# Performance work log

Hardware: AMD Instinct MI355X
Metric: run time of the kernel (lower is better)

The kernel has to match this reference:

```python
import jax, jax.numpy as jnp
import numpy as np

D_MODEL = 1024
NUM_HEADS = 16
HEAD_DIM = D_MODEL // NUM_HEADS
BATCH = 2
SEQ = 2048


def setup_inputs() -> dict:
    key = jax.random.key(0)
    ks = jax.random.split(key, 9)
    s = 1.0 / np.sqrt(D_MODEL)
    inp = {
        "x": jax.random.normal(ks[0], (BATCH, SEQ, D_MODEL), dtype=jnp.float32),
        "mask": jnp.ones((BATCH, SEQ), dtype=jnp.int32),
        "Wq": jax.random.uniform(ks[1], (D_MODEL, D_MODEL), jnp.float32, -s, s),
        "bq": jax.random.uniform(ks[2], (D_MODEL,), jnp.float32, -s, s),
        "Wk": jax.random.uniform(ks[3], (D_MODEL, D_MODEL), jnp.float32, -s, s),
        "bk": jax.random.uniform(ks[4], (D_MODEL,), jnp.float32, -s, s),
        "Wv": jax.random.uniform(ks[5], (D_MODEL, D_MODEL), jnp.float32, -s, s),
        "bv": jax.random.uniform(ks[6], (D_MODEL,), jnp.float32, -s, s),
        "Wo": jax.random.uniform(ks[7], (D_MODEL, D_MODEL), jnp.float32, -s, s),
        "bo": jax.random.uniform(ks[8], (D_MODEL,), jnp.float32, -s, s),
    }
    return inp


def reference(x, mask, Wq, bq, Wk, bk, Wv, bv, Wo, bo):
    B, S, D = x.shape
    H, Hd = NUM_HEADS, HEAD_DIM
    # torch Linear: y = x @ W.T + b ; then reshape to [B, H, S, Hd]
    def proj(W, b):
        return (x @ W.T + b).reshape(B, S, H, Hd).transpose(0, 2, 1, 3)
    Q = proj(Wq, bq)
    K = proj(Wk, bk)
    V = proj(Wv, bv)
    scale = 1.0 / jnp.sqrt(jnp.asarray(Hd, dtype=x.dtype))
    scores = jnp.einsum("bhqd,bhkd->bhqk", Q, K) * scale  # [B,H,S,S]
    # mask [B,S] -> broadcast over query positions; masked_fill(mask==0, -1e9)
    scores = jnp.where(mask[:, None, None, :] == 0, jnp.asarray(-1e9, x.dtype), scores)
    attn = jax.nn.softmax(scores, axis=-1)
    context = jnp.einsum("bhqk,bhkd->bhqd", attn, V)
    context = context.transpose(0, 2, 1, 3).reshape(B, S, D)
    return context @ Wo.T + bo
```

## Files before the change

kernel.cpp:

```cpp
#include <hip/hip_runtime.h>
#include <hip/hip_bf16.h>
#include <cstdint>

#define D_MODEL 1024
#define NUM_HEADS 16
#define HEAD_DIM 64
#define BATCH 2
#define SEQ 2048
#define MROWS (BATCH * SEQ)

typedef __attribute__((ext_vector_type(8))) short bf16x8;
typedef __attribute__((ext_vector_type(4))) float f32x4;
typedef unsigned short u16;

#define QSCALE (0.125f * 1.44269504f)

#if __has_builtin(__builtin_amdgcn_exp2f)
#define EXP2F(x) __builtin_amdgcn_exp2f(x)
#else
#define EXP2F(x) exp2f(x)
#endif

static __device__ __forceinline__ u16 f2bf(float f) {
    unsigned int u = __float_as_uint(f);
    unsigned int lsb = (u >> 16) & 1u;
    u += 0x7fffu + lsb;
    return (u16)(u >> 16);
}

#if __has_builtin(__builtin_amdgcn_cvt_pk_bf16_f32)
static __device__ __forceinline__ unsigned pkbf(float a, float b) {
    typedef __attribute__((ext_vector_type(2))) __bf16 bf2;
    union { bf2 v; unsigned u; } cv;
    cv.v = __builtin_amdgcn_cvt_pk_bf16_f32(a, b);
    return cv.u;
}
#else
static __device__ __forceinline__ unsigned pkbf(float a, float b) {
    unsigned ua = (__float_as_uint(a) + 0x8000u) >> 16;
    unsigned ub = (__float_as_uint(b) + 0x8000u) & 0xffff0000u;
    return ua | ub;
}
#endif

static __device__ __forceinline__ void gload_lds16(const void* g, void* l) {
    __builtin_amdgcn_global_load_lds((const __attribute__((address_space(1))) unsigned int*)g,
                                     (__attribute__((address_space(3))) unsigned int*)l,
                                     16, 0, 0);
}

__global__ void cvt_bf16(const float* __restrict__ src,
                         u16* __restrict__ dst, int n) {
    int i = (blockIdx.x * blockDim.x + threadIdx.x) * 4;
    if (i + 3 < n) {
        float4 v = *(const float4*)(src + i);
        ushort4 o;
        o.x = f2bf(v.x); o.y = f2bf(v.y); o.z = f2bf(v.z); o.w = f2bf(v.w);
        *(ushort4*)(dst + i) = o;
    }
}

__global__ void cvt_bf16_4(const float* __restrict__ s0, const float* __restrict__ s1,
                           const float* __restrict__ s2, const float* __restrict__ s3,
                           u16* __restrict__ dst, int n_each) {
    const int which = blockIdx.y;
    const float* s = (which == 0) ? s0 : (which == 1) ? s1 : (which == 2) ? s2 : s3;
    int i = (blockIdx.x * blockDim.x + threadIdx.x) * 4;
    if (i + 3 < n_each) {
        float4 v = *(const float4*)(s + i);
        ushort4 o;
        o.x = f2bf(v.x); o.y = f2bf(v.y); o.z = f2bf(v.z); o.w = f2bf(v.w);
        *(ushort4*)(dst + (size_t)which * n_each + i) = o;
    }
}

template<int BN, int MODE>
__global__ __launch_bounds__(256, 3)
void gemm_staged(const u16* __restrict__ A, const u16* __restrict__ W,
                 const float* __restrict__ b0, const float* __restrict__ b1,
                 const float* __restrict__ b2,
                 u16* __restrict__ o0, u16* __restrict__ o1, u16* __restrict__ o2,
                 float* __restrict__ of, int K, int N) {
    constexpr int WN = BN / 2;
    constexpr int NJ = WN / 16;
    __shared__ __align__(16) u16 As[128 * 64];
    __shared__ __align__(16) u16 Bs[BN * 64];

    const int lane = threadIdx.x & 63;
    const int w    = threadIdx.x >> 6;
    const int quad = lane >> 4;
    const int l16  = lane & 15;
    const int wm = w >> 1, wn = w & 1;

    const u16* Ablk = A + (size_t)(blockIdx.y * 128) * K;
    const u16* Wblk = W + (size_t)(blockIdx.x * BN) * K;

    const int srow = lane >> 3;
    const int scol = lane & 7;

    f32x4 acc[4][NJ];
#pragma unroll
    for (int i = 0; i < 4; ++i)
#pragma unroll
        for (int j = 0; j < NJ; ++j) acc[i][j] = (f32x4){0.f, 0.f, 0.f, 0.f};

    for (int kb0 = 0; kb0 < K; kb0 += 64) {
        __syncthreads();
#pragma unroll
        for (int t = 0; t < 4; ++t) {
            const int r  = w * 32 + t * 8 + srow;
            const int cg = scol ^ (r & 7);
            gload_lds16(Ablk + (size_t)r * K + kb0 + cg * 8, &As[(w * 32 + t * 8) * 64]);
        }
#pragma unroll
        for (int t = 0; t < BN / 32; ++t) {
            const int r  = w * (BN / 4) + t * 8 + srow;
            const int cg = scol ^ (r & 7);
            gload_lds16(Wblk + (size_t)r * K + kb0 + cg * 8, &Bs[(w * (BN / 4) + t * 8) * 64]);
        }
        __syncthreads();
#pragma unroll
        for (int ks = 0; ks < 2; ++ks) {
            bf16x8 a[4], b[NJ];
#pragma unroll
            for (int i = 0; i < 4; ++i) {
                const int ra = wm * 64 + 16 * i + l16;
                a[i] = *(const bf16x8*)&As[ra * 64 + ((ks * 4 + quad) ^ (ra & 7)) * 8];
            }
#pragma unroll
            for (int j = 0; j < NJ; ++j) {
                const int rb = wn * WN + 16 * j + l16;
                b[j] = *(const bf16x8*)&Bs[rb * 64 + ((ks * 4 + quad) ^ (rb & 7)) * 8];
            }
#pragma unroll
            for (int i = 0; i < 4; ++i)
#pragma unroll
                for (int j = 0; j < NJ; ++j)
                    acc[i][j] = __builtin_amdgcn_mfma_f32_16x16x32_bf16(a[i], b[j], acc[i][j], 0, 0, 0);
        }
    }

    const int mbase = blockIdx.y * 128 + wm * 64;
    const int nbase = blockIdx.x * BN + wn * WN;

    if (MODE == 0) {
#pragma unroll
        for (int j = 0; j < NJ; ++j) {
            const int gn = nbase + 16 * j + l16;
            const int which = gn >> 10, rem = gn & 1023;
            const float bv = (which == 0 ? b0 : which == 1 ? b1 : b2)[rem];
            u16* dst = (which == 0) ? o0 : (which == 1) ? o1 : o2;
            const float scl = (which == 0) ? QSCALE : 1.0f;
            const int h = rem >> 6, d = rem & 63;
#pragma unroll
            for (int i = 0; i < 4; ++i)
#pragma unroll
                for (int r = 0; r < 4; ++r) {
                    const int gm = mbase + 16 * i + quad * 4 + r;
                    const int bb = gm >> 11, s = gm & 2047;
                    dst[(((size_t)(bb * NUM_HEADS + h) * SEQ) + s) * 64 + d] =
                        f2bf((acc[i][j][r] + bv) * scl);
                }
        }
    } else {
#pragma unroll
        for (int j = 0; j < NJ; ++j) {
            const int gn = nbase + 16 * j + l16;
            const float bv = b0[gn];
#pragma unroll
            for (int i = 0; i < 4; ++i)
#pragma unroll
                for (int r = 0; r < 4; ++r) {
                    const int gm = mbase + 16 * i + quad * 4 + r;
                    of[(size_t)gm * N + gn] = acc[i][j][r] + bv;
                }
        }
    }
}

__global__ void transpose_v(const u16* __restrict__ V, u16* __restrict__ VT) {
    __shared__ __align__(16) u16 T[64 * 64];
    const int t    = threadIdx.x;
    const int lane = t & 63, w = t >> 6;
    const int bh   = blockIdx.x & 31, sblk = blockIdx.x >> 5;
    const u16* src = V + ((size_t)bh * SEQ + sblk * 64) * 64;

#pragma unroll
    for (int p = 0; p < 2; ++p) {
        const int r = p * 32 + w * 8 + (lane >> 3);
        const int c = lane & 7;
        bf16x8 v = *(const bf16x8*)(src + r * 64 + c * 8);
        *(bf16x8*)&T[r * 64 + ((c ^ (r & 7)) * 8)] = v;
    }
    __syncthreads();
    u16* dst = VT + ((size_t)bh * 64) * SEQ + sblk * 64;
#pragma unroll
    for (int p = 0; p < 2; ++p) {
        const int r  = p * 32 + w * 8 + (lane >> 3);
        const int sc = lane & 7;
        union { u16 u[8]; bf16x8 v; } pk;
#pragma unroll
        for (int j = 0; j < 8; ++j)
            pk.u[j] = T[(sc * 8 + j) * 64 + (((r >> 3) ^ j) * 8) + (r & 7)];
        *(bf16x8*)(dst + (size_t)r * SEQ + sc * 8) = pk.v;
    }
}

__global__ __launch_bounds__(512, 4)
void attn_kernel(const u16* __restrict__ Q, const u16* __restrict__ K,
                 const u16* __restrict__ VT, const int* __restrict__ mask,
                 u16* __restrict__ ctx) {
    __shared__ __align__(16) u16 Ks[2][64 * 64];
    __shared__ __align__(16) u16 Vs[2][64 * 64];
    __shared__ __align__(16) u16 Ps[8][16 * 72];

    const int lane = threadIdx.x & 63;
    const int w    = threadIdx.x >> 6;
    const int quad = lane >> 4;
    const int l16  = lane & 15;

    const int bh = blockIdx.x & 31;
    const int qb = blockIdx.x >> 5;
    const int b  = bh >> 4;
    const int h  = bh & 15;
    const int qbase = qb * 128 + w * 16;

    const u16* Qh = Q + (size_t)bh * SEQ * 64;
    const u16* Kh = K + (size_t)bh * SEQ * 64;
    const u16* Vh = VT + (size_t)bh * 64 * SEQ;
    const int* mrow = mask + b * SEQ;

    const int srow = lane >> 3;
    const int scol = lane & 7;
    const int cg   = scol ^ srow;

    gload_lds16(Kh + (size_t)(8 * w + srow) * 64 + cg * 8, &Ks[0][(8 * w) * 64]);
    gload_lds16(Vh + (size_t)(8 * w + srow) * SEQ + cg * 8, &Vs[0][(8 * w) * 64]);

    bf16x8 qf[2];
#pragma unroll
    for (int ks = 0; ks < 2; ++ks)
        qf[ks] = *(const bf16x8*)(Qh + (size_t)(qbase + l16) * 64 + 32 * ks + quad * 8);

    f32x4 o[4];
#pragma unroll
    for (int id = 0; id < 4; ++id) o[id] = (f32x4){0.f, 0.f, 0.f, 0.f};
    float lst = 0.f;

    unsigned short* myp = &Ps[w][0];
    const int rowsel = (lane & 48) | (quad * 4);

#pragma unroll 2
    for (int kb = 0; kb < 32; ++kb) {
        const int cur = kb & 1;
        __syncthreads();

        if (kb != 31) {
            const int kn = (kb + 1) * 64;
            gload_lds16(Kh + (size_t)(kn + 8 * w + srow) * 64 + cg * 8,
                        &Ks[cur ^ 1][(8 * w) * 64]);
            gload_lds16(Vh + (size_t)(8 * w + srow) * SEQ + kn + cg * 8,
                        &Vs[cur ^ 1][(8 * w) * 64]);
        }

        const int kstart = kb * 64;
        const int mv = mrow[kstart + lane];
        const bool clean = (__ballot(mv != 0) == ~0ull);

        bf16x8 kf[4][2];
#pragma unroll
        for (int ik = 0; ik < 4; ++ik) {
            const int row = 16 * ik + l16;
#pragma unroll
            for (int ks = 0; ks < 2; ++ks)
                kf[ik][ks] = *(const bf16x8*)&Ks[cur][row * 64 + ((4 * ks + quad) ^ (row & 7)) * 8];
        }

        f32x4 s[4];
#pragma unroll
        for (int ik = 0; ik < 4; ++ik) {
            f32x4 t = (f32x4){0.f, 0.f, 0.f, 0.f};
            t = __builtin_amdgcn_mfma_f32_16x16x32_bf16(kf[ik][0], qf[0], t, 0, 0, 0);
            t = __builtin_amdgcn_mfma_f32_16x16x32_bf16(kf[ik][1], qf[1], t, 0, 0, 0);
            s[ik] = t;
        }

        bf16x8 vf[4][2];
#pragma unroll
        for (int id = 0; id < 4; ++id) {
            const int row = 16 * id + l16;
#pragma unroll
            for (int ks = 0; ks < 2; ++ks)
                vf[id][ks] = *(const bf16x8*)&Vs[cur][row * 64 + ((4 * ks + quad) ^ (row & 7)) * 8];
        }

        if (!clean) {
#pragma unroll
            for (int ik = 0; ik < 4; ++ik) {
                int4 mk = *(const int4*)(mrow + kstart + 16 * ik + quad * 4);
                const int* mp = (const int*)&mk;
#pragma unroll
                for (int r = 0; r < 4; ++r)
                    s[ik][r] = (mp[r] != 0) ? s[ik][r] : -1e9f;
            }
        }

        float rs = 0.f;
#pragma unroll
        for (int ik = 0; ik < 4; ++ik) {
            const float p0 = EXP2F(fminf(s[ik][0], 80.f));
            const float p1 = EXP2F(fminf(s[ik][1], 80.f));
            const float p2 = EXP2F(fminf(s[ik][2], 80.f));
            const float p3 = EXP2F(fminf(s[ik][3], 80.f));
            rs += (p0 + p1) + (p2 + p3);
            uint2 pk;
            pk.x = pkbf(p0, p1);
            pk.y = pkbf(p2, p3);
            *(uint2*)(myp + l16 * 72 + 16 * ik + quad * 4) = pk;
        }
        rs += __shfl_xor(rs, 16, 64);
        rs += __shfl_xor(rs, 32, 64);
        lst += rs;

#pragma unroll
        for (int ks = 0; ks < 2; ++ks) {
            bf16x8 pf = *(const bf16x8*)(myp + l16 * 72 + 32 * ks + quad * 8);
#pragma unroll
            for (int id = 0; id < 4; ++id)
                o[id] = __builtin_amdgcn_mfma_f32_16x16x32_bf16(pf, vf[id][ks], o[id], 0, 0, 0);
        }
    }

    float linv[4];
#pragma unroll
    for (int r = 0; r < 4; ++r) linv[r] = 1.f / __shfl(lst, rowsel + r, 64);
#pragma unroll
    for (int id = 0; id < 4; ++id)
#pragma unroll
        for (int r = 0; r < 4; ++r) {
            const int q = qbase + quad * 4 + r;
            const int d = 16 * id + l16;
            ctx[((size_t)(b * SEQ + q)) * D_MODEL + h * 64 + d] = f2bf(o[id][r] * linv[r]);
        }
}

extern "C" void kernel_launch(void* const* d_in, const int* in_sizes, int n_in,
                              void* d_out, int out_size, void* d_ws, size_t ws_size,
                              hipStream_t stream) {
    const float* x    = (const float*)d_in[0];
    const int*   mask = (const int*)d_in[1];
    const float* Wq   = (const float*)d_in[2];
    const float* bq   = (const float*)d_in[3];
    const float* Wk   = (const float*)d_in[4];
    const float* bk   = (const float*)d_in[5];
    const float* Wv   = (const float*)d_in[6];
    const float* bv   = (const float*)d_in[7];
    const float* Wo   = (const float*)d_in[8];
    const float* bo   = (const float*)d_in[9];

    u16* xb  = (u16*)d_ws;
    u16* wqb = xb  + (size_t)MROWS * D_MODEL;
    u16* wkb = wqb + (size_t)D_MODEL * D_MODEL;
    u16* wvb = wkb + (size_t)D_MODEL * D_MODEL;
    u16* wob = wvb + (size_t)D_MODEL * D_MODEL;
    u16* Qb  = wob + (size_t)D_MODEL * D_MODEL;
    u16* Kb  = Qb  + (size_t)MROWS * D_MODEL;
    u16* VTb = Kb  + (size_t)MROWS * D_MODEL;
    u16* ctx = VTb + (size_t)MROWS * D_MODEL;

    const int nx = MROWS * D_MODEL;
    const int nw = D_MODEL * D_MODEL;
    cvt_bf16<<<nx / 1024, 256, 0, stream>>>(x, xb, nx);
    cvt_bf16_4<<<dim3(nw / 1024, 4), 256, 0, stream>>>(Wq, Wk, Wv, Wo, wqb, nw);

    gemm_staged<128, 0><<<dim3(3 * D_MODEL / 128, MROWS / 128), 256, 0, stream>>>(
        xb, wqb, bq, bk, bv, Qb, Kb, ctx, nullptr, D_MODEL, 3 * D_MODEL);

    transpose_v<<<BATCH * NUM_HEADS * (SEQ / 64), 256, 0, stream>>>(ctx, VTb);

    attn_kernel<<<BATCH * NUM_HEADS * (SEQ / 128), 512, 0, stream>>>(Qb, Kb, VTb, mask, ctx);

    gemm_staged<64, 1><<<dim3(D_MODEL / 64, MROWS / 128), 256, 0, stream>>>(
        ctx, wob, bo, nullptr, nullptr, nullptr, nullptr, nullptr,
        (float*)d_out, D_MODEL, D_MODEL);
}
```

Baseline: 203.6 us.

## Fuse V transpose into QKV GEMM epilogue and merge conversion launches

The QKV projection GEMM now writes V directly in transposed [B,H,D,S] layout by staging the V-tile accumulators through a padded LDS buffer and emitting coalesced 16-byte row stores, which removes the separate transpose_v kernel and its round trip through global memory. The two fp32-to-bf16 conversion kernels are merged into one launch over a 2D grid covering x and all four weight matrices. In exchange, every GEMM instantiation carries an extra 17 KB of shared memory, which may reduce occupancy, and the V blocks add two block-wide barriers to their epilogue.

```diff
diff --git a/kernel.cpp b/kernel.cpp
--- a/kernel.cpp
+++ b/kernel.cpp
@@ -49,29 +49,24 @@
                                      16, 0, 0);
 }
 
-__global__ void cvt_bf16(const float* __restrict__ src,
-                         u16* __restrict__ dst, int n) {
-    int i = (blockIdx.x * blockDim.x + threadIdx.x) * 4;
-    if (i + 3 < n) {
-        float4 v = *(const float4*)(src + i);
-        ushort4 o;
-        o.x = f2bf(v.x); o.y = f2bf(v.y); o.z = f2bf(v.z); o.w = f2bf(v.w);
-        *(ushort4*)(dst + i) = o;
-    }
-}
-
-__global__ void cvt_bf16_4(const float* __restrict__ s0, const float* __restrict__ s1,
-                           const float* __restrict__ s2, const float* __restrict__ s3,
-                           u16* __restrict__ dst, int n_each) {
+__global__ void cvt_all(const float* __restrict__ x,
+                        const float* __restrict__ w0, const float* __restrict__ w1,
+                        const float* __restrict__ w2, const float* __restrict__ w3,
+                        u16* __restrict__ base) {
     const int which = blockIdx.y;
-    const float* s = (which == 0) ? s0 : (which == 1) ? s1 : (which == 2) ? s2 : s3;
-    int i = (blockIdx.x * blockDim.x + threadIdx.x) * 4;
-    if (i + 3 < n_each) {
-        float4 v = *(const float4*)(s + i);
-        ushort4 o;
-        o.x = f2bf(v.x); o.y = f2bf(v.y); o.z = f2bf(v.z); o.w = f2bf(v.w);
-        *(ushort4*)(dst + (size_t)which * n_each + i) = o;
-    }
+    const int NE = D_MODEL * D_MODEL;
+    const float* s;
+    if (which < 4)      s = x + (size_t)which * NE;
+    else if (which == 4) s = w0;
+    else if (which == 5) s = w1;
+    else if (which == 6) s = w2;
+    else                 s = w3;
+    u16* dst = base + (size_t)which * NE;
+    const int i = (blockIdx.x * blockDim.x + threadIdx.x) * 4;
+    float4 v = *(const float4*)(s + i);
+    ushort4 o;
+    o.x = f2bf(v.x); o.y = f2bf(v.y); o.z = f2bf(v.z); o.w = f2bf(v.w);
+    *(ushort4*)(dst + i) = o;
 }
 
 template<int BN, int MODE>
@@ -85,6 +80,7 @@
     constexpr int NJ = WN / 16;
     __shared__ __align__(16) u16 As[128 * 64];
     __shared__ __align__(16) u16 Bs[BN * 64];
+    __shared__ __align__(16) u16 T[64 * 136];
 
     const int lane = threadIdx.x & 63;
     const int w    = threadIdx.x >> 6;
@@ -143,13 +139,50 @@
     const int mbase = blockIdx.y * 128 + wm * 64;
     const int nbase = blockIdx.x * BN + wn * WN;
 
+    if (MODE == 0 && blockIdx.x >= 16) {
+        const int mb    = blockIdx.y * 128;
+        const int bb    = mb >> 11;
+        const int sbase = mb & 2047;
+#pragma unroll
+        for (int p = 0; p < 2; ++p) {
+            __syncthreads();
+            if (wn == p) {
+#pragma unroll
+                for (int j = 0; j < NJ; ++j) {
+                    const int nl = 16 * j + l16;
+                    const float bv = b2[(nbase + 16 * j + l16) & 1023];
+#pragma unroll
+                    for (int i = 0; i < 4; ++i) {
+                        const int ml = wm * 64 + 16 * i + quad * 4;
+                        uint2 pk;
+                        pk.x = pkbf(acc[i][j][0] + bv, acc[i][j][1] + bv);
+                        pk.y = pkbf(acc[i][j][2] + bv, acc[i][j][3] + bv);
+                        *(uint2*)&T[nl * 136 + ml] = pk;
+                    }
+                }
+            }
+            __syncthreads();
+            const int row = threadIdx.x >> 2;
+            const int gn2 = blockIdx.x * 128 + p * 64 + row;
+            const int rem2 = gn2 & 1023;
+            const int h = rem2 >> 6, d = rem2 & 63;
+            u16* dstrow = o2 + (((size_t)(bb * NUM_HEADS + h) * 64) + d) * SEQ + sbase;
+#pragma unroll
+            for (int k = 0; k < 4; ++k) {
+                const int chunk = (threadIdx.x & 3) * 4 + k;
+                *(uint4*)(dstrow + chunk * 8) = *(const uint4*)&T[row * 136 + chunk * 8];
+            }
+        }
+        return;
+    }
+
     if (MODE == 0) {
 #pragma unroll
         for (int j = 0; j < NJ; ++j) {
             const int gn = nbase + 16 * j + l16;
             const int which = gn >> 10, rem = gn & 1023;
-            const float bv = (which == 0 ? b0 : which == 1 ? b1 : b2)[rem];
-            u16* dst = (which == 0) ? o0 : (which == 1) ? o1 : o2;
+            const float bv = (which == 0 ? b0 : b1)[rem];
+            u16* dst = (which == 0) ? o0 : o1;
             const float scl = (which == 0) ? QSCALE : 1.0f;
             const int h = rem >> 6, d = rem & 63;
 #pragma unroll
@@ -175,34 +208,6 @@
                     of[(size_t)gm * N + gn] = acc[i][j][r] + bv;
                 }
         }
-    }
-}
-
-__global__ void transpose_v(const u16* __restrict__ V, u16* __restrict__ VT) {
-    __shared__ __align__(16) u16 T[64 * 64];
-    const int t    = threadIdx.x;
-    const int lane = t & 63, w = t >> 6;
-    const int bh   = blockIdx.x & 31, sblk = blockIdx.x >> 5;
-    const u16* src = V + ((size_t)bh * SEQ + sblk * 64) * 64;
-
-#pragma unroll
-    for (int p = 0; p < 2; ++p) {
-        const int r = p * 32 + w * 8 + (lane >> 3);
-        const int c = lane & 7;
-        bf16x8 v = *(const bf16x8*)(src + r * 64 + c * 8);
-        *(bf16x8*)&T[r * 64 + ((c ^ (r & 7)) * 8)] = v;
-    }
-    __syncthreads();
-    u16* dst = VT + ((size_t)bh * 64) * SEQ + sblk * 64;
-#pragma unroll
-    for (int p = 0; p < 2; ++p) {
-        const int r  = p * 32 + w * 8 + (lane >> 3);
-        const int sc = lane & 7;
-        union { u16 u[8]; bf16x8 v; } pk;
-#pragma unroll
-        for (int j = 0; j < 8; ++j)
-            pk.u[j] = T[(sc * 8 + j) * 64 + (((r >> 3) ^ j) * 8) + (r & 7)];
-        *(bf16x8*)(dst + (size_t)r * SEQ + sc * 8) = pk.v;
     }
 }
 
@@ -360,23 +365,17 @@
 
     u16* xb  = (u16*)d_ws;
     u16* wqb = xb  + (size_t)MROWS * D_MODEL;
-    u16* wkb = wqb + (size_t)D_MODEL * D_MODEL;
-    u16* wvb = wkb + (size_t)D_MODEL * D_MODEL;
-    u16* wob = wvb + (size_t)D_MODEL * D_MODEL;
+    u16* wob = wqb + (size_t)3 * D_MODEL * D_MODEL;
     u16* Qb  = wob + (size_t)D_MODEL * D_MODEL;
     u16* Kb  = Qb  + (size_t)MROWS * D_MODEL;
     u16* VTb = Kb  + (size_t)MROWS * D_MODEL;
     u16* ctx = VTb + (size_t)MROWS * D_MODEL;
 
-    const int nx = MROWS * D_MODEL;
-    const int nw = D_MODEL * D_MODEL;
-    cvt_bf16<<<nx / 1024, 256, 0, stream>>>(x, xb, nx);
-    cvt_bf16_4<<<dim3(nw / 1024, 4), 256, 0, stream>>>(Wq, Wk, Wv, Wo, wqb, nw);
+    cvt_all<<<dim3(D_MODEL * D_MODEL / 1024, 8), 256, 0, stream>>>(
+        x, Wq, Wk, Wv, Wo, xb);
 
     gemm_staged<128, 0><<<dim3(3 * D_MODEL / 128, MROWS / 128), 256, 0, stream>>>(
-        xb, wqb, bq, bk, bv, Qb, Kb, ctx, nullptr, D_MODEL, 3 * D_MODEL);
-
-    transpose_v<<<BATCH * NUM_HEADS * (SEQ / 64), 256, 0, stream>>>(ctx, VTb);
+        xb, wqb, bq, bk, bv, Qb, Kb, VTb, nullptr, D_MODEL, 3 * D_MODEL);
 
     attn_kernel<<<BATCH * NUM_HEADS * (SEQ / 128), 512, 0, stream>>>(Qb, Kb, VTb, mask, ctx);
 
```

After: 189.5 us. 1.07x faster.
